# Kernel tuning notes

Hardware: AMD Instinct MI355X
Metric: run time of the kernel (lower is better)

Reference implementation:

```python
import jax, jax.numpy as jnp
import numpy as np
from jax import lax

B, C, H, W, G = 16, 256, 96, 96, 16


def setup_inputs() -> dict:
    key = jax.random.key(0)
    ks = jax.random.split(key, 8)
    return {
        "x": jax.random.normal(ks[0], (B, C, H, W), jnp.float32),
        "in_w": jax.random.normal(ks[1], (C, C), jnp.float32) / np.sqrt(C).astype(np.float32),
        "gn1_w": jnp.ones((C,), jnp.float32),
        "gn1_b": jnp.zeros((C,), jnp.float32),
        "a_p": jnp.zeros((4, C), jnp.float32),   # torch init: zeros -> sigmoid = 0.5
        "b_p": jnp.ones((4, C), jnp.float32),
        "c_p": jnp.ones((4, C), jnp.float32),
        "d_p": jnp.ones((4, C), jnp.float32),
        "gate_w": jax.random.normal(ks[2], (C, C), jnp.float32) / np.sqrt(C).astype(np.float32),
        "gate_b": jnp.zeros((C,), jnp.float32),
        "dw_w": jax.random.normal(ks[3], (C, 1, 3, 3), jnp.float32) / 3.0,  # depthwise 3x3
        "pw_w": jax.random.normal(ks[4], (C, C), jnp.float32) / np.sqrt(C).astype(np.float32),
        "gn2_w": jnp.ones((C,), jnp.float32),
        "gn2_b": jnp.zeros((C,), jnp.float32),
    }


def group_norm(x, w, b, groups=G, eps=1e-5):
    Bn, Cn, Hn, Wn = x.shape
    xg = x.reshape(Bn, groups, Cn // groups, Hn, Wn)
    mu = xg.mean((2, 3, 4), keepdims=True)
    var = xg.var((2, 3, 4), keepdims=True)  # biased, matches torch GroupNorm
    xn = ((xg - mu) * lax.rsqrt(var + eps)).reshape(Bn, Cn, Hn, Wn)
    return xn * w[None, :, None, None] + b[None, :, None, None]


def scan_seq(seq, a, b, c, d):
    # seq: [N, C, L].  h_t = a*h_{t-1} + b*x_t ; y_t = c*h_t + d*x_t
    xs = jnp.moveaxis(seq, -1, 0)  # [L, N, C]
    def step(h, x_t):
        h = a * h + b * x_t
        return h, c * h + d * x_t
    h0 = jnp.zeros(xs.shape[1:], seq.dtype)
    _, ys = lax.scan(step, h0, xs)
    return jnp.moveaxis(ys, 0, -1)  # [N, C, L]


def scan_w(x, reverse, a, b, c, d):
    if reverse:
        x = x[:, :, :, ::-1]
    Bn, Cn, Hn, Wn = x.shape
    seq = x.transpose(0, 2, 1, 3).reshape(Bn * Hn, Cn, Wn)
    y = scan_seq(seq, a, b, c, d).reshape(Bn, Hn, Cn, Wn).transpose(0, 2, 1, 3)
    return y[:, :, :, ::-1] if reverse else y


def scan_h(x, reverse, a, b, c, d):
    if reverse:
        x = x[:, :, ::-1, :]
    Bn, Cn, Hn, Wn = x.shape
    seq = x.transpose(0, 3, 1, 2).reshape(Bn * Wn, Cn, Hn)
    y = scan_seq(seq, a, b, c, d).reshape(Bn, Wn, Cn, Hn).transpose(0, 2, 3, 1)
    return y[:, :, ::-1, :] if reverse else y


def reference(x, in_w, gn1_w, gn1_b, a_p, b_p, c_p, d_p, gate_w, gate_b, dw_w, pw_w, gn2_w, gn2_b):
    # in_proj: 1x1 conv (no bias) -> GroupNorm -> SiLU
    xp = jnp.einsum('oc,bchw->bohw', in_w, x)
    xp = jax.nn.silu(group_norm(xp, gn1_w, gn1_b))
    # 4-directional per-channel linear recurrences
    a = jax.nn.sigmoid(a_p)
    lr = scan_w(xp, False, a[0], b_p[0], c_p[0], d_p[0])
    rl = scan_w(xp, True,  a[1], b_p[1], c_p[1], d_p[1])
    tb = scan_h(xp, False, a[2], b_p[2], c_p[2], d_p[2])
    bt = scan_h(xp, True,  a[3], b_p[3], c_p[3], d_p[3])
    gate = jax.nn.sigmoid(jnp.einsum('oc,bchw->bohw', gate_w, xp) + gate_b[None, :, None, None])
    fused = 0.25 * (lr + rl + tb + bt) * gate
    # out_proj: depthwise 3x3 -> 1x1 conv -> GroupNorm -> SiLU
    dw = lax.conv_general_dilated(fused, dw_w, (1, 1), 'SAME',
                                  dimension_numbers=('NCHW', 'OIHW', 'NCHW'),
                                  feature_group_count=fused.shape[1])
    out = jnp.einsum('oc,bchw->bohw', pw_w, dw)
    return jax.nn.silu(group_norm(out, gn2_w, gn2_b))
```

## Files before the change

kernel.cpp:

```cpp
#include <hip/hip_runtime.h>
#include <hip/hip_bf16.h>

#define Bx 16
#define Cx 256
#define Hx 96
#define Wx 96
#define HWx 9216
#define NTOK 147456
#define Gx 16
#define GRPN 147456.0f

typedef unsigned short u16;
typedef unsigned int u32;
typedef __attribute__((ext_vector_type(8))) short short8;
typedef __attribute__((ext_vector_type(4))) float float4_;
typedef __attribute__((ext_vector_type(4))) unsigned short us4;
typedef __attribute__((ext_vector_type(8))) unsigned short us8;
typedef __attribute__((ext_vector_type(4))) unsigned int ui4;

__device__ __forceinline__ float b2f(u16 u){ u32 x = ((u32)u)<<16; float f; __builtin_memcpy(&f,&x,4); return f; }
__device__ __forceinline__ u16 f2b(float f){ u32 x; __builtin_memcpy(&x,&f,4); x += 0x7FFFu + ((x>>16)&1u); return (u16)(x>>16); }
__device__ __forceinline__ float sigm(float v){ return 1.0f/(1.0f+__expf(-v)); }

__global__ __launch_bounds__(256) void k_transpose(const float* __restrict__ X, u16* __restrict__ XT){
  __shared__ u16 tile[32][36];
  int blk = blockIdx.x;
  int ct  = blk & 7;
  int hwt = (blk >> 3) % 288;
  int b   = blk / 2304;
  int c0 = ct*32, hw0 = hwt*32;
  int t = threadIdx.x;
  int r  = t >> 3;
  int q4 = (t & 7) << 2;
  float4_ v = *(const float4_*)&X[((size_t)(b*Cx + c0 + r))*HWx + hw0 + q4];
  tile[r][q4+0]=f2b(v[0]); tile[r][q4+1]=f2b(v[1]); tile[r][q4+2]=f2b(v[2]); tile[r][q4+3]=f2b(v[3]);
  __syncthreads();
  us4 o = { tile[q4+0][r], tile[q4+1][r], tile[q4+2][r], tile[q4+3][r] };
  *(us4*)&XT[((size_t)(b*HWx + hw0 + r))*Cx + c0 + q4] = o;
}

#define BM 128
#define BN 64
#define LDA 40
#define LDB 264

template<int MODE>
__global__ __launch_bounds__(256) void k_gemm(const u16* __restrict__ A,
                                              const float* __restrict__ Wm,
                                              u16* __restrict__ Y,
                                              float* __restrict__ stats,
                                              const float* __restrict__ bias,
                                              u16* __restrict__ Sb)
{
  __shared__ u16 Ws[BN*LDB];
  __shared__ u16 As[BM*LDA];
  __shared__ float red[4][16][2];
  const int tid = threadIdx.x;
  const int n0 = blockIdx.x * BM;
  const int o0 = blockIdx.y * BN;
  #pragma unroll
  for (int it=0; it<16; ++it){
    int cid = tid + it*256;
    int row = cid >> 6;
    int ko  = (cid & 63) << 2;
    float4_ w4 = *(const float4_*)&Wm[(size_t)(o0+row)*Cx + ko];
    us4 wb = { f2b(w4[0]), f2b(w4[1]), f2b(w4[2]), f2b(w4[3]) };
    *(us4*)&Ws[row*LDB + ko] = wb;
  }
  const int lane = tid & 63;
  const int wid  = tid >> 6;
  const int lm   = lane & 15;
  const int quad = lane >> 4;
  const int wn = wid & 1;
  const int wo = wid >> 1;
  float4_ acc[4][2];
  #pragma unroll
  for (int i=0;i<4;++i){ acc[i][0] = (float4_)0.0f; acc[i][1] = (float4_)0.0f; }
  for (int kk=0; kk<Cx; kk+=32){
    __syncthreads();
    #pragma unroll
    for (int it=0; it<2; ++it){
      int cid = tid + it*256;
      int r = cid >> 2;
      int ko = (cid & 3) << 3;
      *(ui4*)&As[r*LDA + ko] = *(const ui4*)&A[(size_t)(n0+r)*Cx + kk + ko];
    }
    __syncthreads();
    short8 af[4], bf[2];
    #pragma unroll
    for (int i=0;i<4;++i) af[i] = *(const short8*)&As[(wn*64 + i*16 + lm)*LDA + quad*8];
    #pragma unroll
    for (int j=0;j<2;++j) bf[j] = *(const short8*)&Ws[(wo*32 + j*16 + lm)*LDB + kk + quad*8];
    #pragma unroll
    for (int i=0;i<4;++i)
      #pragma unroll
      for (int j=0;j<2;++j)
        acc[i][j] = __builtin_amdgcn_mfma_f32_16x16x32_bf16(af[i], bf[j], acc[i][j], 0, 0, 0);
  }
  const int b = n0 / HWx;
  if (MODE == 1){
    #pragma unroll
    for (int i=0;i<4;++i){
      #pragma unroll
      for (int j=0;j<2;++j){
        int oc = o0 + wo*32 + j*16 + lm;
        float bb = bias[oc];
        #pragma unroll
        for (int r=0;r<4;++r){
          int row = n0 + wn*64 + i*16 + quad*4 + r;
          size_t idx = (size_t)row*Cx + oc;
          float g = sigm(acc[i][j][r] + bb);
          Y[idx] = f2b(0.25f * b2f(Sb[idx]) * g);
        }
      }
    }
  } else {
    float s0=0,s1=0,q0=0,q1=0;
    #pragma unroll
    for (int i=0;i<4;++i){
      #pragma unroll
      for (int j=0;j<2;++j){
        int oc = o0 + wo*32 + j*16 + lm;
        #pragma unroll
        for (int r=0;r<4;++r){
          int row = n0 + wn*64 + i*16 + quad*4 + r;
          float v = acc[i][j][r];
          Y[(size_t)row*Cx + oc] = f2b(v);
          if (j==0){ s0+=v; q0+=v*v; } else { s1+=v; q1+=v*v; }
        }
      }
    }
    s0 += __shfl_xor(s0,16); s0 += __shfl_xor(s0,32);
    q0 += __shfl_xor(q0,16); q0 += __shfl_xor(q0,32);
    s1 += __shfl_xor(s1,16); s1 += __shfl_xor(s1,32);
    q1 += __shfl_xor(q1,16); q1 += __shfl_xor(q1,32);
    if (tid < 128) ((float*)red)[tid] = 0.0f;
    __syncthreads();
    if (lane < 16){
      atomicAdd(&red[wo*2+0][lm][0], s0);
      atomicAdd(&red[wo*2+0][lm][1], q0);
      atomicAdd(&red[wo*2+1][lm][0], s1);
      atomicAdd(&red[wo*2+1][lm][1], q1);
    }
    __syncthreads();
    if (tid < 4){
      float ss=0, qq=0;
      #pragma unroll
      for (int k=0;k<16;++k){ ss += red[tid][k][0]; qq += red[tid][k][1]; }
      int g = (o0 >> 4) + tid;
      atomicAdd(&stats[(b*Gx + g)*2 + 0], ss);
      atomicAdd(&stats[(b*Gx + g)*2 + 1], qq);
    }
  }
}

__global__ void k_finalize(const float* __restrict__ st, float* __restrict__ mr){
  int i = threadIdx.x;
  float s = st[i*2+0], q = st[i*2+1];
  float mu  = s * (1.0f/GRPN);
  float var = q * (1.0f/GRPN) - mu*mu;
  mr[i*2+0] = mu;
  mr[i*2+1] = rsqrtf(var + 1e-5f);
}

__global__ __launch_bounds__(256) void k_norm_silu(const u16* __restrict__ Yin, u16* __restrict__ Xp,
    const float* __restrict__ mr, const float* __restrict__ gw, const float* __restrict__ gb){
  size_t e8 = ((size_t)blockIdx.x*256 + threadIdx.x)*8;
  int c = (int)(e8 & 255);
  int b = (int)(e8 / ((size_t)HWx*Cx));
  int g = c >> 4;
  float mu = mr[(b*Gx+g)*2], rs = mr[(b*Gx+g)*2+1];
  us8 v = *(const us8*)&Yin[e8];
  us8 o;
  #pragma unroll
  for (int k=0;k<8;++k){
    float xn = (b2f(v[k]) - mu)*rs*gw[c+k] + gb[c+k];
    o[k] = f2b(xn * sigm(xn));
  }
  *(us8*)&Xp[e8] = o;
}

__global__ __launch_bounds__(128) void k_scan_w(const u16* __restrict__ Xp, u16* __restrict__ S,
    const float* __restrict__ ap, const float* __restrict__ bp, const float* __restrict__ cpr, const float* __restrict__ dp){
  __shared__ u16 ins[96*128];
  __shared__ u16 accs[96*128];
  int blk = blockIdx.x;
  int ch = blk & 1;
  int row = blk >> 1;
  int h = row % Hx, b = row / Hx;
  int t = threadIdx.x;
  int c = ch*128 + t;
  float A0 = sigm(ap[c]),      B0 = bp[c],      C0 = cpr[c],      D0 = dp[c];
  float A1 = sigm(ap[Cx+c]),   B1 = bp[Cx+c],   C1 = cpr[Cx+c],   D1 = dp[Cx+c];
  const u16* base = Xp + ((size_t)(b*Hx + h)*Wx)*Cx + c;
  for (int w=0; w<Wx; ++w) ins[w*128+t] = base[(size_t)w*Cx];
  float hs = 0.0f;
  #pragma unroll 4
  for (int w=0; w<Wx; ++w){
    float xv = b2f(ins[w*128+t]);
    hs = A0*hs + B0*xv;
    accs[w*128+t] = f2b(C0*hs + D0*xv);
  }
  hs = 0.0f;
  u16* sb = S + ((size_t)(b*Hx + h)*Wx)*Cx + c;
  #pragma unroll 4
  for (int w=Wx-1; w>=0; --w){
    float xv = b2f(ins[w*128+t]);
    hs = A1*hs + B1*xv;
    sb[(size_t)w*Cx] = f2b(C1*hs + D1*xv + b2f(accs[w*128+t]));
  }
}

__global__ __launch_bounds__(128) void k_scan_h(const u16* __restrict__ Xp, u16* __restrict__ S,
    const float* __restrict__ ap, const float* __restrict__ bp, const float* __restrict__ cpr, const float* __restrict__ dp){
  __shared__ u16 ins[96*128];
  __shared__ u16 accs[96*128];
  int blk = blockIdx.x;
  int ch = blk & 1;
  int col = blk >> 1;
  int w = col % Wx, b = col / Wx;
  int t = threadIdx.x;
  int c = ch*128 + t;
  float A2 = sigm(ap[2*Cx+c]), B2 = bp[2*Cx+c], C2 = cpr[2*Cx+c], D2 = dp[2*Cx+c];
  float A3 = sigm(ap[3*Cx+c]), B3 = bp[3*Cx+c], C3 = cpr[3*Cx+c], D3 = dp[3*Cx+c];
  const u16* base = Xp + ((size_t)(b*Hx)*Wx + w)*Cx + c;
  for (int h=0; h<Hx; ++h) ins[h*128+t] = base[(size_t)h*Wx*Cx];
  float hs = 0.0f;
  #pragma unroll 4
  for (int h=0; h<Hx; ++h){
    float xv = b2f(ins[h*128+t]);
    hs = A2*hs + B2*xv;
    accs[h*128+t] = f2b(C2*hs + D2*xv);
  }
  hs = 0.0f;
  u16* sb = S + ((size_t)(b*Hx)*Wx + w)*Cx + c;
  #pragma unroll 4
  for (int h=Hx-1; h>=0; --h){
    float xv = b2f(ins[h*128+t]);
    hs = A3*hs + B3*xv;
    size_t off = (size_t)h*Wx*Cx;
    sb[off] = f2b(C3*hs + D3*xv + b2f(accs[h*128+t]) + b2f(sb[off]));
  }
}

__global__ __launch_bounds__(256) void k_dwconv(const u16* __restrict__ F, const float* __restrict__ dwW, u16* __restrict__ O){
  __shared__ float wl[2304];
  int t = threadIdx.x;
  #pragma unroll
  for (int i=0;i<9;++i) wl[t + i*256] = dwW[t + i*256];
  __syncthreads();
  int blk = blockIdx.x;
  int w16 = blk % (Wx/16);
  int h   = (blk/(Wx/16)) % Hx;
  int b   = blk / ((Wx/16)*Hx);
  int cq = (t & 63) << 2;
  int w0 = (w16 << 4) + ((t >> 6) << 2);
  float wt[36];
  #pragma unroll
  for (int j=0;j<9;++j) *(float4_*)&wt[4*j] = *(const float4_*)&wl[cq*9 + 4*j];
  float acc[4][4];
  #pragma unroll
  for (int ow=0;ow<4;++ow){ acc[ow][0]=0.0f; acc[ow][1]=0.0f; acc[ow][2]=0.0f; acc[ow][3]=0.0f; }
  const u16* Fb = F + ((size_t)(b*Hx)*Wx)*Cx + cq;
  #pragma unroll
  for (int ky=0; ky<3; ++ky){
    int hh = h + ky - 1;
    if (hh < 0 || hh >= Hx) continue;
    #pragma unroll
    for (int j=0; j<6; ++j){
      int ww = w0 + j - 1;
      if (ww < 0 || ww >= Wx) continue;
      us4 v = *(const us4*)&Fb[((size_t)hh*Wx + ww)*Cx];
      float f0=b2f(v[0]), f1=b2f(v[1]), f2=b2f(v[2]), f3=b2f(v[3]);
      #pragma unroll
      for (int ow = (j-2<0?0:j-2); ow <= (j<3?j:3); ++ow){
        int kidx = ky*3 + (j - ow);
        acc[ow][0] += f0 * wt[0*9 + kidx];
        acc[ow][1] += f1 * wt[1*9 + kidx];
        acc[ow][2] += f2 * wt[2*9 + kidx];
        acc[ow][3] += f3 * wt[3*9 + kidx];
      }
    }
  }
  #pragma unroll
  for (int ow=0; ow<4; ++ow){
    us4 o = { f2b(acc[ow][0]), f2b(acc[ow][1]), f2b(acc[ow][2]), f2b(acc[ow][3]) };
    *(us4*)&O[((size_t)((b*Hx+h)*Wx) + w0 + ow)*Cx + cq] = o;
  }
}

__global__ __launch_bounds__(256) void k_norm_tr(const u16* __restrict__ Y3, float* __restrict__ Out,
    const float* __restrict__ mr, const float* __restrict__ gw, const float* __restrict__ gb){
  __shared__ float tile[32][36];
  int blk = blockIdx.x;
  int ct  = blk & 7;
  int hwt = (blk >> 3) % 288;
  int b   = blk / 2304;
  int c0 = ct*32, hw0 = hwt*32;
  int t = threadIdx.x;
  int r  = t >> 3;
  int q4 = (t & 7) << 2;
  us4 v = *(const us4*)&Y3[((size_t)(b*HWx + hw0 + r))*Cx + c0 + q4];
  int g = (c0 + q4) >> 4;
  float mu = mr[(b*Gx+g)*2], rs = mr[(b*Gx+g)*2+1];
  #pragma unroll
  for (int i=0;i<4;++i){
    float xn = (b2f(v[i]) - mu)*rs*gw[c0+q4+i] + gb[c0+q4+i];
    tile[r][q4+i] = xn * sigm(xn);
  }
  __syncthreads();
  float4_ o = { tile[q4+0][r], tile[q4+1][r], tile[q4+2][r], tile[q4+3][r] };
  *(float4_*)&Out[((size_t)(b*Cx + c0 + r))*HWx + hw0 + q4] = o;
}

extern "C" void kernel_launch(void* const* d_in, const int* in_sizes, int n_in,
                              void* d_out, int out_size, void* d_ws, size_t ws_size,
                              hipStream_t stream){
  (void)in_sizes; (void)n_in; (void)out_size; (void)ws_size;
  const float* x    = (const float*)d_in[0];
  const float* in_w = (const float*)d_in[1];
  const float* gn1w = (const float*)d_in[2];
  const float* gn1b = (const float*)d_in[3];
  const float* ap   = (const float*)d_in[4];
  const float* bp   = (const float*)d_in[5];
  const float* cp   = (const float*)d_in[6];
  const float* dp   = (const float*)d_in[7];
  const float* gw   = (const float*)d_in[8];
  const float* gb   = (const float*)d_in[9];
  const float* dww  = (const float*)d_in[10];
  const float* pww  = (const float*)d_in[11];
  const float* gn2w = (const float*)d_in[12];
  const float* gn2b = (const float*)d_in[13];
  float* out = (float*)d_out;
  char* ws = (char*)d_ws;
  const size_t NB = (size_t)NTOK * Cx * 2;
  u16* xT = (u16*)(ws);
  u16* y1 = (u16*)(ws + NB);
  u16* xp = (u16*)(ws + 2*NB);
  u16* S  = (u16*)(ws + 3*NB);
  float* stats1 = (float*)(ws + 4*NB);
  float* stats2 = stats1 + 512;
  float* mr1    = stats1 + 1024;
  float* mr2    = stats1 + 1536;

  hipMemsetAsync(stats1, 0, 1024*sizeof(float), stream);

  k_transpose<<<36864, 256, 0, stream>>>(x, xT);
  k_gemm<0><<<dim3(NTOK/BM, Cx/BN), 256, 0, stream>>>(xT, in_w, y1, stats1, nullptr, nullptr);
  k_finalize<<<1, 256, 0, stream>>>(stats1, mr1);
  k_norm_silu<<<NTOK*Cx/2048, 256, 0, stream>>>(y1, xp, mr1, gn1w, gn1b);
  k_scan_w<<<Bx*Hx*2, 128, 0, stream>>>(xp, S, ap, bp, cp, dp);
  k_scan_h<<<Bx*Wx*2, 128, 0, stream>>>(xp, S, ap, bp, cp, dp);
  k_gemm<1><<<dim3(NTOK/BM, Cx/BN), 256, 0, stream>>>(xp, gw, S, nullptr, gb, S);
  k_dwconv<<<Bx*Hx*(Wx/16), 256, 0, stream>>>(S, dww, xT);
  k_gemm<0><<<dim3(NTOK/BM, Cx/BN), 256, 0, stream>>>(xT, pww, y1, stats2, nullptr, nullptr);
  k_finalize<<<1, 256, 0, stream>>>(stats2, mr2);
  k_norm_tr<<<36864, 256, 0, stream>>>(y1, out, mr2, gn2w, gn2b);
}
```

Measured before the change: 763.4 us.

## Fuse GroupNorm+SiLU into row scan and swizzle GEMM block order

Removes the standalone norm+SiLU pass by applying it inside k_scan_w. That kernel reads y1, normalizes, keeps the result in shared memory for its scan and also writes xp for the later scan_h and gate GEMM, which saves one full read of y1 and one kernel launch. The GEMM launches also change to a 1D grid with an XCD-style swizzle, so the 4 output-channel tiles of a token block land on the same XCD and share A-tile reuse in L2. The risk is that the per-element writes to xp in scan_w are strided per channel, which could reduce coalescing compared with the vectorized norm kernel.

After: 752.6 us. About the same (-1.4%).

```diff
diff --git a/kernel.cpp b/kernel.cpp
--- a/kernel.cpp
+++ b/kernel.cpp
@@ -56,8 +56,10 @@
   __shared__ u16 As[BM*LDA];
   __shared__ float red[4][16][2];
   const int tid = threadIdx.x;
-  const int n0 = blockIdx.x * BM;
-  const int o0 = blockIdx.y * BN;
+  int lin = blockIdx.x;
+  int swz = (lin & 7) * 576 + (lin >> 3);
+  const int n0 = (swz >> 2) * BM;
+  const int o0 = (swz & 3) * BN;
   #pragma unroll
   for (int it=0; it<16; ++it){
     int cid = tid + it*256;
@@ -163,25 +165,9 @@
   mr[i*2+1] = rsqrtf(var + 1e-5f);
 }
 
-__global__ __launch_bounds__(256) void k_norm_silu(const u16* __restrict__ Yin, u16* __restrict__ Xp,
-    const float* __restrict__ mr, const float* __restrict__ gw, const float* __restrict__ gb){
-  size_t e8 = ((size_t)blockIdx.x*256 + threadIdx.x)*8;
-  int c = (int)(e8 & 255);
-  int b = (int)(e8 / ((size_t)HWx*Cx));
-  int g = c >> 4;
-  float mu = mr[(b*Gx+g)*2], rs = mr[(b*Gx+g)*2+1];
-  us8 v = *(const us8*)&Yin[e8];
-  us8 o;
-  #pragma unroll
-  for (int k=0;k<8;++k){
-    float xn = (b2f(v[k]) - mu)*rs*gw[c+k] + gb[c+k];
-    o[k] = f2b(xn * sigm(xn));
-  }
-  *(us8*)&Xp[e8] = o;
-}
-
-__global__ __launch_bounds__(128) void k_scan_w(const u16* __restrict__ Xp, u16* __restrict__ S,
-    const float* __restrict__ ap, const float* __restrict__ bp, const float* __restrict__ cpr, const float* __restrict__ dp){
+__global__ __launch_bounds__(128) void k_scan_w(const u16* __restrict__ Y1, u16* __restrict__ Xp, u16* __restrict__ S,
+    const float* __restrict__ ap, const float* __restrict__ bp, const float* __restrict__ cpr, const float* __restrict__ dp,
+    const float* __restrict__ mr, const float* __restrict__ gwv, const float* __restrict__ gbv){
   __shared__ u16 ins[96*128];
   __shared__ u16 accs[96*128];
   int blk = blockIdx.x;
@@ -192,8 +178,17 @@
   int c = ch*128 + t;
   float A0 = sigm(ap[c]),      B0 = bp[c],      C0 = cpr[c],      D0 = dp[c];
   float A1 = sigm(ap[Cx+c]),   B1 = bp[Cx+c],   C1 = cpr[Cx+c],   D1 = dp[Cx+c];
-  const u16* base = Xp + ((size_t)(b*Hx + h)*Wx)*Cx + c;
-  for (int w=0; w<Wx; ++w) ins[w*128+t] = base[(size_t)w*Cx];
+  int g = c >> 4;
+  float mu = mr[(b*Gx+g)*2], rs = mr[(b*Gx+g)*2+1];
+  float gwc = gwv[c], gbc = gbv[c];
+  const u16* base = Y1 + ((size_t)(b*Hx + h)*Wx)*Cx + c;
+  u16* xpb = Xp + ((size_t)(b*Hx + h)*Wx)*Cx + c;
+  for (int w=0; w<Wx; ++w){
+    float xn = (b2f(base[(size_t)w*Cx]) - mu)*rs*gwc + gbc;
+    u16 v = f2b(xn * sigm(xn));
+    ins[w*128+t] = v;
+    xpb[(size_t)w*Cx] = v;
+  }
   float hs = 0.0f;
   #pragma unroll 4
   for (int w=0; w<Wx; ++w){
@@ -346,14 +341,13 @@
   hipMemsetAsync(stats1, 0, 1024*sizeof(float), stream);
 
   k_transpose<<<36864, 256, 0, stream>>>(x, xT);
-  k_gemm<0><<<dim3(NTOK/BM, Cx/BN), 256, 0, stream>>>(xT, in_w, y1, stats1, nullptr, nullptr);
+  k_gemm<0><<<4608, 256, 0, stream>>>(xT, in_w, y1, stats1, nullptr, nullptr);
   k_finalize<<<1, 256, 0, stream>>>(stats1, mr1);
-  k_norm_silu<<<NTOK*Cx/2048, 256, 0, stream>>>(y1, xp, mr1, gn1w, gn1b);
-  k_scan_w<<<Bx*Hx*2, 128, 0, stream>>>(xp, S, ap, bp, cp, dp);
+  k_scan_w<<<Bx*Hx*2, 128, 0, stream>>>(y1, xp, S, ap, bp, cp, dp, mr1, gn1w, gn1b);
   k_scan_h<<<Bx*Wx*2, 128, 0, stream>>>(xp, S, ap, bp, cp, dp);
-  k_gemm<1><<<dim3(NTOK/BM, Cx/BN), 256, 0, stream>>>(xp, gw, S, nullptr, gb, S);
+  k_gemm<1><<<4608, 256, 0, stream>>>(xp, gw, S, nullptr, gb, S);
   k_dwconv<<<Bx*Hx*(Wx/16), 256, 0, stream>>>(S, dww, xT);
-  k_gemm<0><<<dim3(NTOK/BM, Cx/BN), 256, 0, stream>>>(xT, pww, y1, stats2, nullptr, nullptr);
+  k_gemm<0><<<4608, 256, 0, stream>>>(xT, pww, y1, stats2, nullptr, nullptr);
   k_finalize<<<1, 256, 0, stream>>>(stats2, mr2);
   k_norm_tr<<<36864, 256, 0, stream>>>(y1, out, mr2, gn2w, gn2b);
 }
```
